# Optimization experiments

Measured on AMD Instinct MI355X. Metric: run time of the kernel, lower is better.

Reference implementation:

```python
import jax, jax.numpy as jnp
import numpy as np
import math

C = 256
NUM_GROUPS = 8
EPS = 1e-5


def group_norm(x, scale, bias):
    # x: (B, C, H, W)
    B, Cc, H, W = x.shape
    g = x.reshape(B, NUM_GROUPS, Cc // NUM_GROUPS, H, W)
    mean = g.mean(axis=(2, 3, 4), keepdims=True)
    var = g.var(axis=(2, 3, 4), keepdims=True)
    g = (g - mean) * jax.lax.rsqrt(var + EPS)
    x = g.reshape(B, Cc, H, W)
    return x * scale[None, :, None, None] + bias[None, :, None, None]


def setup_inputs() -> dict:
    key = jax.random.key(0)
    ks = jax.random.split(key, 6)
    B, H, W = 4, 64, 64
    s = 1.0 / math.sqrt(C)
    return {
        "input": jax.random.normal(ks[0], (B, C, H, W), dtype=jnp.float32),
        "gn_scale": jnp.ones((C,), jnp.float32),
        "gn_bias": jnp.zeros((C,), jnp.float32),
        "Wq": jax.random.normal(ks[1], (C, C), jnp.float32) * s,
        "bq": jnp.zeros((C,), jnp.float32),
        "Wk": jax.random.normal(ks[2], (C, C), jnp.float32) * s,
        "bk": jnp.zeros((C,), jnp.float32),
        "Wv": jax.random.normal(ks[3], (C, C), jnp.float32) * s,
        "bv": jnp.zeros((C,), jnp.float32),
        "Wo": jax.random.normal(ks[4], (C, C), jnp.float32) * s,
        "bo": jnp.zeros((C,), jnp.float32),
    }


def reference(input, gn_scale, gn_bias, Wq, bq, Wk, bk, Wv, bv, Wo, bo):
    B, Cc, H, W = input.shape
    N = H * W
    h = group_norm(input, gn_scale, gn_bias)          # (B,C,H,W)
    hf = h.reshape(B, Cc, N)                          # (B,C,N)
    # 1x1 convs are per-pixel linear maps: out[c] = W[c,c'] h[c'] + b[c]
    q = jnp.einsum('oc,bcn->bon', Wq, hf) + bq[None, :, None]
    k = jnp.einsum('oc,bcn->bon', Wk, hf) + bk[None, :, None]
    v = jnp.einsum('oc,bcn->bon', Wv, hf) + bv[None, :, None]
    # attention: scores (B,N,N) = q^T k / sqrt(C)
    attn = jnp.einsum('bcn,bcm->bnm', q, k) / jnp.sqrt(jnp.float32(Cc))
    attn = jax.nn.softmax(attn, axis=-1)
    # output = value @ attention^T -> (B,C,N)
    out = jnp.einsum('bcm,bnm->bcn', v, attn)
    out = out.reshape(B, Cc, H, W)
    out = jnp.einsum('oc,bchw->bohw', Wo, out) + bo[None, :, None, None]
    return input + out
```

## Files before the change

kernel.cpp:

```cpp
#include <hip/hip_runtime.h>
#include <hip/hip_bf16.h>
#include <stdint.h>

#define BATCH 4
#define CH 256
#define NPIX 4096
#define NGROUP 8
#define GCH 32
#define EPSV 1e-5f

typedef __attribute__((ext_vector_type(8))) short bf16x8;
typedef __attribute__((ext_vector_type(4))) float f32x4;
typedef __attribute__((ext_vector_type(16))) float f32x16;

#define MFMA_B16(a, b, c) __builtin_amdgcn_mfma_f32_16x16x32_bf16((a), (b), (c), 0, 0, 0)
#define MFMA32(a, b, c)   __builtin_amdgcn_mfma_f32_32x32x16_bf16((a), (b), (c), 0, 0, 0)

#define GLOAD16(gsrc, ldst)                                                        \
  __builtin_amdgcn_global_load_lds(                                               \
      (const __attribute__((address_space(1))) uint32_t*)(gsrc),                  \
      (__attribute__((address_space(3))) uint32_t*)(ldst), 16, 0, 0)

__device__ __forceinline__ unsigned short f2bf(float f) {
  union { float f; uint32_t u; } v; v.f = f;
  return (unsigned short)((v.u + 0x7FFFu + ((v.u >> 16) & 1u)) >> 16);
}
__device__ __forceinline__ float bf2f(unsigned short h) {
  union { uint32_t u; float f; } v; v.u = ((uint32_t)h) << 16;
  return v.f;
}

#define QSCALE 0.09016813306f

__global__ __launch_bounds__(256) void wconv(
    const float* __restrict__ Wq, const float* __restrict__ Wk,
    const float* __restrict__ Wv, const float* __restrict__ Wo,
    const float* __restrict__ bq,
    unsigned short* __restrict__ Wq_b, unsigned short* __restrict__ Wk_b,
    unsigned short* __restrict__ Wv_b, unsigned short* __restrict__ Wo_b,
    float* __restrict__ bq_s) {
  int i = blockIdx.x * 256 + threadIdx.x;
  Wq_b[i] = f2bf(Wq[i] * QSCALE);
  Wk_b[i] = f2bf(Wk[i]);
  Wv_b[i] = f2bf(Wv[i]);
  Wo_b[i] = f2bf(Wo[i]);
  if (i < CH) bq_s[i] = bq[i] * QSCALE;
}

__global__ __launch_bounds__(256) void gn_stats(const float* __restrict__ x,
                                                float* __restrict__ part) {
  int bc = blockIdx.x;
  const float* row = x + (size_t)bc * NPIX;
  int t = threadIdx.x;
  float s = 0.f, ss = 0.f;
  #pragma unroll
  for (int i = 0; i < 4; ++i) {
    f32x4 v = *(const f32x4*)(row + (i * 256 + t) * 4);
    s += v[0] + v[1] + v[2] + v[3];
    ss += v[0]*v[0] + v[1]*v[1] + v[2]*v[2] + v[3]*v[3];
  }
  #pragma unroll
  for (int m = 1; m < 64; m <<= 1) { s += __shfl_xor(s, m); ss += __shfl_xor(ss, m); }
  __shared__ float ls[8];
  if ((t & 63) == 0) { ls[(t >> 6) * 2] = s; ls[(t >> 6) * 2 + 1] = ss; }
  __syncthreads();
  if (t == 0) {
    part[bc * 2]     = ls[0] + ls[2] + ls[4] + ls[6];
    part[bc * 2 + 1] = ls[1] + ls[3] + ls[5] + ls[7];
  }
}

__global__ __launch_bounds__(256) void gn_apply(
    const float* __restrict__ x, const float* __restrict__ part,
    const float* __restrict__ gamma, const float* __restrict__ beta,
    unsigned short* __restrict__ h_t) {
  int chunk = blockIdx.x, g = blockIdx.y, b = blockIdx.z;
  int t = threadIdx.x;
  __shared__ float s_mean, s_rstd;
  __shared__ unsigned short tile[GCH][72];
  if (t == 0) {
    float S = 0.f, SS = 0.f;
    const float* p = part + (size_t)(b * CH + g * GCH) * 2;
    for (int j = 0; j < GCH; ++j) { S += p[2 * j]; SS += p[2 * j + 1]; }
    float inv = 1.0f / (float)(GCH * NPIX);
    float mean = S * inv;
    float var = SS * inv - mean * mean;
    s_mean = mean;
    s_rstd = rsqrtf(var + EPSV);
  }
  __syncthreads();
  float mean = s_mean, rstd = s_rstd;
  int n0 = chunk * 64;
  int p = t & 63;
  int csub = t >> 6;
  #pragma unroll
  for (int cl = 0; cl < GCH; cl += 4) {
    int c = cl + csub;
    float val = x[(size_t)(b * CH + g * GCH + c) * NPIX + n0 + p];
    float gm = gamma[g * GCH + c], bt = beta[g * GCH + c];
    tile[c][p] = f2bf((val - mean) * rstd * gm + bt);
  }
  __syncthreads();
  int pix = t >> 2, cc = (t & 3) * 8;
  bf16x8 vv;
  #pragma unroll
  for (int j = 0; j < 8; ++j) vv[j] = (short)tile[cc + j][pix];
  *(bf16x8*)(h_t + (size_t)(b * NPIX + n0 + pix) * CH + g * GCH + cc) = vv;
}

template <int BIAS_COL, int RESID, int OUT_BF16>
__global__ __launch_bounds__(256, 2) void gemm_bt_k(
    const unsigned short* __restrict__ A, const unsigned short* __restrict__ Bt,
    void* __restrict__ Cout, const float* __restrict__ bias,
    const float* __restrict__ resid, int M, int N,
    long aStride, long btStride, long cStride) {
  __shared__ __align__(16) unsigned short a_lds[128 * 64];
  __shared__ __align__(16) unsigned short b_lds[128 * 64];

  const int bz = blockIdx.z;
  const char* Ac = (const char*)(A + (size_t)bz * aStride);
  const char* Bc = (const char*)(Bt + (size_t)bz * btStride);
  const int m0 = blockIdx.x * 128;
  const int n0 = blockIdx.y * 128;
  const int t = threadIdx.x;
  const int w = t >> 6, l = t & 63, lr = l & 15, lk = l >> 4;
  const int wr = (w >> 1) * 64, wc = (w & 1) * 64;

  f32x4 acc[4][4];
  #pragma unroll
  for (int i = 0; i < 4; ++i)
    #pragma unroll
    for (int j = 0; j < 4; ++j) acc[i][j] = f32x4{0.f, 0.f, 0.f, 0.f};

  char* alc = (char*)a_lds;
  char* blc = (char*)b_lds;

  for (int kt = 0; kt < 4; ++kt) {
    __syncthreads();
    #pragma unroll
    for (int i = 0; i < 4; ++i) {
      int base = i * 4096 + w * 1024;
      int lin = base + l * 16;
      int sw = lin ^ (((lin >> 7) & 7) << 4);
      int row = lin >> 7;
      int inr = sw & 127;
      GLOAD16(Ac + (size_t)(m0 + row) * 512 + kt * 128 + inr, alc + base);
      GLOAD16(Bc + (size_t)(n0 + row) * 512 + kt * 128 + inr, blc + base);
    }
    __syncthreads();
    #pragma unroll
    for (int ks = 0; ks < 2; ++ks) {
      bf16x8 af[4], bf[4];
      #pragma unroll
      for (int f = 0; f < 4; ++f) {
        int ra = wr + f * 16 + lr;
        int la = ra * 128 + ks * 64 + lk * 16;
        af[f] = *(const bf16x8*)(alc + (la ^ ((ra & 7) << 4)));
        int rb = wc + f * 16 + lr;
        int lb = rb * 128 + ks * 64 + lk * 16;
        bf[f] = *(const bf16x8*)(blc + (lb ^ ((rb & 7) << 4)));
      }
      #pragma unroll
      for (int mf = 0; mf < 4; ++mf)
        #pragma unroll
        for (int nf = 0; nf < 4; ++nf)
          acc[mf][nf] = MFMA_B16(af[mf], bf[nf], acc[mf][nf]);
    }
  }

  #pragma unroll
  for (int mf = 0; mf < 4; ++mf) {
    #pragma unroll
    for (int nf = 0; nf < 4; ++nf) {
      int col = n0 + wc + nf * 16 + lr;
      #pragma unroll
      for (int r = 0; r < 4; ++r) {
        int row = m0 + wr + mf * 16 + lk * 4 + r;
        float val = acc[mf][nf][r];
        val += BIAS_COL ? bias[col] : bias[row];
        size_t idx = (size_t)bz * (size_t)cStride + (size_t)row * N + col;
        if (RESID) val += resid[idx];
        if (OUT_BF16) ((unsigned short*)Cout)[idx] = f2bf(val);
        else          ((float*)Cout)[idx] = val;
      }
    }
  }
}

#define KSPLIT 4
#define KRANGE (NPIX / KSPLIT)
#define KBLK 32
#define NT (KRANGE / KBLK)

__global__ __launch_bounds__(256, 2) void flash_kernel(
    const unsigned short* __restrict__ q_t, const unsigned short* __restrict__ k_t,
    const unsigned short* __restrict__ v,
    unsigned short* __restrict__ p0, unsigned short* __restrict__ p1,
    unsigned short* __restrict__ p2, unsigned short* __restrict__ p3,
    float* __restrict__ ml) {
  __shared__ __align__(16) unsigned short k_lds[2][KBLK * CH];
  __shared__ __align__(16) unsigned short v_lds[2][CH * KBLK];

  const int F = blockIdx.x;
  const int bid = (F >> 3) + ((F & 7) << 6);
  const int qx = bid & 31, b = (bid >> 5) & 3, ksp = bid >> 7;
  const int q0 = qx * 128;
  const int t = threadIdx.x;
  const int w = t >> 6, l = t & 63;
  const int l31 = l & 31, hi = l >> 5;

  bf16x8 qf[16];
  {
    const char* qp = (const char*)(q_t + (size_t)(b * NPIX + q0 + w * 32 + l31) * CH);
    #pragma unroll
    for (int ds = 0; ds < 16; ++ds)
      qf[ds] = *(const bf16x8*)(qp + ds * 32 + hi * 16);
  }

  f32x16 oacc[8];
  #pragma unroll
  for (int cf = 0; cf < 8; ++cf)
    #pragma unroll
    for (int r = 0; r < 16; ++r) oacc[cf][r] = 0.f;
  float m_run = -3e38f, l_run = 0.f;
  uint32_t pkc[8];
  #pragma unroll
  for (int m = 0; m < 8; ++m) pkc[m] = 0;

  const char* kg = (const char*)(k_t + ((size_t)b * NPIX + ksp * KRANGE) * CH);
  const char* vg = (const char*)(v + (size_t)b * CH * NPIX + ksp * KRANGE);

  int koffb[4], voffb[4], ldsd[4];
  #pragma unroll
  for (int i_ = 0; i_ < 4; ++i_) {
    int d = i_ * 4096 + w * 1024 + l * 16;
    ldsd[i_] = d;
    int r_ = d >> 9;
    int c_ = ((d >> 4) & 31) ^ r_;
    koffb[i_] = r_ * 512 + (c_ << 4);
    voffb[i_] = ((c_ >> 2) * 32 + r_) * (NPIX * 2) + ((c_ & 3) << 4);
  }

  #define STAGE_K(buf, tt)                                                         \
    { _Pragma("unroll")                                                            \
      for (int i_ = 0; i_ < 4; ++i_)                                               \
        GLOAD16(kg + (size_t)koffb[i_] + (size_t)(tt) * (KBLK * 512),              \
                (char*)k_lds[buf] + ldsd[i_]); }
  #define STAGE_V(buf, tt)                                                         \
    { _Pragma("unroll")                                                            \
      for (int i_ = 0; i_ < 4; ++i_)                                               \
        GLOAD16(vg + (size_t)voffb[i_] + (size_t)(tt) * (KBLK * 2),                \
                (char*)v_lds[buf] + ldsd[i_]); }

  auto do_pv = [&](const char* vlcx) {
    #pragma unroll
    for (int s = 0; s < 2; ++s) {
      uint32_t own0 = hi ? pkc[4 * s + 2] : pkc[4 * s + 0];
      uint32_t own1 = hi ? pkc[4 * s + 3] : pkc[4 * s + 1];
      uint32_t snd0 = hi ? pkc[4 * s + 0] : pkc[4 * s + 2];
      uint32_t snd1 = hi ? pkc[4 * s + 1] : pkc[4 * s + 3];
      uint32_t rcv0 = (uint32_t)__shfl_xor((int)snd0, 32);
      uint32_t rcv1 = (uint32_t)__shfl_xor((int)snd1, 32);
      union { uint32_t u[4]; bf16x8 v8; } apu;
      apu.u[0] = hi ? rcv0 : own0;
      apu.u[1] = hi ? rcv1 : own1;
      apu.u[2] = hi ? own0 : rcv0;
      apu.u[3] = hi ? own1 : rcv1;
      bf16x8 ap = apu.v8;
      #pragma unroll
      for (int cf = 0; cf < 8; ++cf) {
        bf16x8 bv = *(const bf16x8*)(
            vlcx + l31 * 512 + ((((cf << 2) + (s << 1) + hi) ^ l31) << 4));
        oacc[cf] = MFMA32(ap, bv, oacc[cf]);
      }
    }
  };

  STAGE_K(0, 0);
  STAGE_K(1, 1);
  STAGE_V(0, 0);
  asm volatile("s_waitcnt vmcnt(8)" ::: "memory");
  __builtin_amdgcn_s_barrier();

  for (int u = 0; u < NT; ++u) {
    const char* klc = (const char*)k_lds[u & 1];
    const char* vlc = (const char*)v_lds[(u ^ 1) & 1];

    __builtin_amdgcn_s_setprio(1);
    if (u > 0) do_pv(vlc);
    f32x16 sacc;
    #pragma unroll
    for (int r = 0; r < 16; ++r) sacc[r] = 0.f;
    #pragma unroll
    for (int ds = 0; ds < 16; ++ds) {
      bf16x8 kf = *(const bf16x8*)(klc + l31 * 512 + ((((ds << 1) + hi) ^ l31) << 4));
      sacc = MFMA32(kf, qf[ds], sacc);
    }
    __builtin_amdgcn_s_setprio(0);

    float mx[8];
    #pragma unroll
    for (int r = 0; r < 8; ++r) mx[r] = fmaxf(sacc[r], sacc[r + 8]);
    #pragma unroll
    for (int st = 4; st >= 1; st >>= 1)
      #pragma unroll
      for (int r = 0; r < 4; ++r)
        if (r < st) mx[r] = fmaxf(mx[r], mx[r + st]);
    float tm = fmaxf(mx[0], __shfl_xor(mx[0], 32));

    if (!__all(tm <= m_run + 6.f)) {
      float mn = fmaxf(m_run, tm);
      float al = exp2f(m_run - mn);
      m_run = mn;
      l_run *= al;
      #pragma unroll
      for (int r = 0; r < 16; ++r) {
        float alr = __shfl(al, (r & 3) + 8 * (r >> 2) + 4 * hi);
        #pragma unroll
        for (int cf = 0; cf < 8; ++cf) oacc[cf][r] *= alr;
      }
    }

    float psp[4] = {0.f, 0.f, 0.f, 0.f};
    #pragma unroll
    for (int m = 0; m < 8; ++m) {
      float pa = exp2f(sacc[2 * m] - m_run);
      float pb = exp2f(sacc[2 * m + 1] - m_run);
      psp[m & 3] += pa + pb;
      union { __hip_bfloat162 h2; uint32_t u; } cv;
      cv.h2 = __float22bfloat162_rn(make_float2(pa, pb));
      pkc[m] = cv.u;
    }
    float ps = (psp[0] + psp[1]) + (psp[2] + psp[3]);
    ps += __shfl_xor(ps, 32);
    l_run += ps;

    asm volatile("" ::: "memory");
    __builtin_amdgcn_s_barrier();
    if (u + 2 < NT) STAGE_K((u & 1), u + 2);
    if (u + 1 < NT) STAGE_V(((u + 1) & 1), u + 1);
    if (u + 2 < NT)      { asm volatile("s_waitcnt vmcnt(8)" ::: "memory"); }
    else if (u + 1 < NT) { asm volatile("s_waitcnt vmcnt(4)" ::: "memory"); }
    else                 { asm volatile("s_waitcnt vmcnt(0)" ::: "memory"); }
    __builtin_amdgcn_s_barrier();
  }

  __builtin_amdgcn_s_setprio(1);
  do_pv((const char*)v_lds[(NT - 1) & 1]);
  __builtin_amdgcn_s_setprio(0);

  {
    unsigned short* opart = (ksp == 0) ? p0 : (ksp == 1) ? p1 : (ksp == 2) ? p2 : p3;
    unsigned short* op = opart + (size_t)(b * NPIX + q0 + w * 32) * CH;
    #pragma unroll
    for (int cf = 0; cf < 8; ++cf)
      #pragma unroll
      for (int r = 0; r < 16; ++r)
        op[(size_t)((r & 3) + 8 * (r >> 2) + 4 * hi) * CH + cf * 32 + l31] =
            f2bf(oacc[cf][r]);
    if (l < 32) {
      float* mlrow = ml + ((size_t)ksp * (BATCH * NPIX) +
                           b * NPIX + q0 + w * 32 + l) * 2;
      mlrow[0] = m_run;
      mlrow[1] = l_run;
    }
  }
  #undef STAGE_K
  #undef STAGE_V
}

__global__ __launch_bounds__(256) void flash_merge(
    const unsigned short* __restrict__ p0, unsigned short* __restrict__ p1io,
    const unsigned short* __restrict__ p2, const unsigned short* __restrict__ p3,
    const float* __restrict__ ml) {
  const int R = BATCH * NPIX;
  int t = threadIdx.x;
  int gr = blockIdx.x * 16 + (t >> 4);
  int colg = (t & 15) * 16;
  float m0 = ml[(size_t)gr * 2],           l0 = ml[(size_t)gr * 2 + 1];
  float m1 = ml[((size_t)R + gr) * 2],     l1 = ml[((size_t)R + gr) * 2 + 1];
  float m2 = ml[((size_t)2 * R + gr) * 2], l2 = ml[((size_t)2 * R + gr) * 2 + 1];
  float m3 = ml[((size_t)3 * R + gr) * 2], l3 = ml[((size_t)3 * R + gr) * 2 + 1];
  float m = fmaxf(fmaxf(m0, m1), fmaxf(m2, m3));
  float e0 = exp2f(m0 - m), e1 = exp2f(m1 - m);
  float e2 = exp2f(m2 - m), e3 = exp2f(m3 - m);
  float inv = 1.0f / (e0 * l0 + e1 * l1 + e2 * l2 + e3 * l3);
  const bf16x8* a0 = (const bf16x8*)(p0 + (size_t)gr * CH + colg);
  bf16x8*       a1 = (bf16x8*)(p1io + (size_t)gr * CH + colg);
  const bf16x8* a2 = (const bf16x8*)(p2 + (size_t)gr * CH + colg);
  const bf16x8* a3 = (const bf16x8*)(p3 + (size_t)gr * CH + colg);
  #pragma unroll
  for (int h = 0; h < 2; ++h) {
    bf16x8 v0 = a0[h], v1 = a1[h], v2 = a2[h], v3 = a3[h], o;
    #pragma unroll
    for (int j = 0; j < 8; ++j)
      o[j] = (short)f2bf((e0 * bf2f((unsigned short)v0[j]) +
                          e1 * bf2f((unsigned short)v1[j]) +
                          e2 * bf2f((unsigned short)v2[j]) +
                          e3 * bf2f((unsigned short)v3[j])) * inv);
    a1[h] = o;
  }
}

extern "C" void kernel_launch(void* const* d_in, const int* in_sizes, int n_in,
                              void* d_out, int out_size, void* d_ws, size_t ws_size,
                              hipStream_t stream) {
  const float* x   = (const float*)d_in[0];
  const float* gsc = (const float*)d_in[1];
  const float* gbi = (const float*)d_in[2];
  const float* Wq  = (const float*)d_in[3];
  const float* bq  = (const float*)d_in[4];
  const float* Wk  = (const float*)d_in[5];
  const float* bk  = (const float*)d_in[6];
  const float* Wv  = (const float*)d_in[7];
  const float* bv  = (const float*)d_in[8];
  const float* Wo  = (const float*)d_in[9];
  const float* bo  = (const float*)d_in[10];

  char* ws = (char*)d_ws;
  unsigned short* Wq_b = (unsigned short*)(ws);
  unsigned short* Wk_b = (unsigned short*)(ws + 131072);
  unsigned short* Wv_b = (unsigned short*)(ws + 262144);
  unsigned short* Wo_b = (unsigned short*)(ws + 393216);
  float* bq_s          = (float*)(ws + 524288);
  float* part          = (float*)(ws + 525312);
  char* big            = ws + 533504;
  unsigned short* h_t  = (unsigned short*)(big);
  unsigned short* q_t  = (unsigned short*)(big + 1 * 8388608ull);
  unsigned short* k_t  = (unsigned short*)(big + 2 * 8388608ull);
  unsigned short* v_   = (unsigned short*)(big + 3 * 8388608ull);
  unsigned short* o_t  = (unsigned short*)(big + 4 * 8388608ull);
  float* ml            = (float*)(big + 5 * 8388608ull);
  if (ws_size < 533504 + 5ull * 8388608ull + 524288ull) return;

  unsigned short* dout_u = (unsigned short*)d_out;
  unsigned short* op2 = dout_u;
  unsigned short* op3 = dout_u + 4194304;

  wconv<<<256, 256, 0, stream>>>(Wq, Wk, Wv, Wo, bq, Wq_b, Wk_b, Wv_b, Wo_b, bq_s);
  gn_stats<<<BATCH * CH, 256, 0, stream>>>(x, part);
  gn_apply<<<dim3(64, NGROUP, BATCH), 256, 0, stream>>>(x, part, gsc, gbi, h_t);

  gemm_bt_k<1, 0, 1><<<dim3(128, 2, 1), 256, 0, stream>>>(
      h_t, Wq_b, q_t, bq_s, nullptr, 16384, 256, 0, 0, 0);
  gemm_bt_k<1, 0, 1><<<dim3(128, 2, 1), 256, 0, stream>>>(
      h_t, Wk_b, k_t, bk, nullptr, 16384, 256, 0, 0, 0);
  gemm_bt_k<0, 0, 1><<<dim3(2, 32, BATCH), 256, 0, stream>>>(
      Wv_b, h_t, v_, bv, nullptr, 256, 4096, 0, 1048576, 1048576);

  flash_kernel<<<dim3(32 * BATCH * KSPLIT, 1, 1), 256, 0, stream>>>(
      q_t, k_t, v_, h_t, o_t, op2, op3, ml);
  flash_merge<<<(BATCH * NPIX) / 16, 256, 0, stream>>>(h_t, o_t, op2, op3, ml);

  gemm_bt_k<0, 1, 0><<<dim3(2, 32, BATCH), 256, 0, stream>>>(
      Wo_b, o_t, (float*)d_out, bo, x, 256, 4096, 0, 1048576, 1048576);
}
```

Baseline: 146.7 us.

## Fuse Q and K projections into one GEMM and restructure flash loop

The Q and K projection GEMMs become a single launch over a 512-wide output whose epilogue splits columns between the q_t and k_t buffers. The bias is a concatenated scaled-q/k vector built in wconv. In the flash kernel, the per-lane swizzled LDS offsets are precomputed into registers. The main loop is unrolled by two with compile-time buffer indices, and the PV pass uses packed bf16 P fragments built at the end of each iteration rather than shuffling at the start of the next. This aims to cut one launch, reuse the A-tile reads of h_t, and reduce address arithmetic in the hot loop, at the cost of more live registers.

```diff
diff --git a/kernel.cpp b/kernel.cpp
--- a/kernel.cpp
+++ b/kernel.cpp
@@ -35,16 +35,19 @@
 __global__ __launch_bounds__(256) void wconv(
     const float* __restrict__ Wq, const float* __restrict__ Wk,
     const float* __restrict__ Wv, const float* __restrict__ Wo,
-    const float* __restrict__ bq,
+    const float* __restrict__ bq, const float* __restrict__ bk,
     unsigned short* __restrict__ Wq_b, unsigned short* __restrict__ Wk_b,
     unsigned short* __restrict__ Wv_b, unsigned short* __restrict__ Wo_b,
-    float* __restrict__ bq_s) {
+    float* __restrict__ bqk_s) {
   int i = blockIdx.x * 256 + threadIdx.x;
   Wq_b[i] = f2bf(Wq[i] * QSCALE);
   Wk_b[i] = f2bf(Wk[i]);
   Wv_b[i] = f2bf(Wv[i]);
   Wo_b[i] = f2bf(Wo[i]);
-  if (i < CH) bq_s[i] = bq[i] * QSCALE;
+  if (i < CH) {
+    bqk_s[i] = bq[i] * QSCALE;
+    bqk_s[CH + i] = bk[i];
+  }
 }
 
 __global__ __launch_bounds__(256) void gn_stats(const float* __restrict__ x,
@@ -108,12 +111,12 @@
   *(bf16x8*)(h_t + (size_t)(b * NPIX + n0 + pix) * CH + g * GCH + cc) = vv;
 }
 
-template <int BIAS_COL, int RESID, int OUT_BF16>
+template <int BIAS_COL, int RESID, int OUT_BF16, int SPLIT>
 __global__ __launch_bounds__(256, 2) void gemm_bt_k(
     const unsigned short* __restrict__ A, const unsigned short* __restrict__ Bt,
     void* __restrict__ Cout, const float* __restrict__ bias,
     const float* __restrict__ resid, int M, int N,
-    long aStride, long btStride, long cStride) {
+    long aStride, long btStride, long cStride, void* __restrict__ Cout2) {
   __shared__ __align__(16) unsigned short a_lds[128 * 64];
   __shared__ __align__(16) unsigned short b_lds[128 * 64];
 
@@ -178,10 +181,16 @@
         int row = m0 + wr + mf * 16 + lk * 4 + r;
         float val = acc[mf][nf][r];
         val += BIAS_COL ? bias[col] : bias[row];
-        size_t idx = (size_t)bz * (size_t)cStride + (size_t)row * N + col;
-        if (RESID) val += resid[idx];
-        if (OUT_BF16) ((unsigned short*)Cout)[idx] = f2bf(val);
-        else          ((float*)Cout)[idx] = val;
+        if (SPLIT) {
+          unsigned short* dst = (col < 256) ? (unsigned short*)Cout
+                                            : (unsigned short*)Cout2;
+          dst[(size_t)row * 256 + (col & 255)] = f2bf(val);
+        } else {
+          size_t idx = (size_t)bz * (size_t)cStride + (size_t)row * N + col;
+          if (RESID) val += resid[idx];
+          if (OUT_BF16) ((unsigned short*)Cout)[idx] = f2bf(val);
+          else          ((float*)Cout)[idx] = val;
+        }
       }
     }
   }
@@ -217,15 +226,18 @@
       qf[ds] = *(const bf16x8*)(qp + ds * 32 + hi * 16);
   }
 
+  uint32_t xoff[16];
+  #pragma unroll
+  for (int j = 0; j < 16; ++j)
+    xoff[j] = (uint32_t)(l31 * 512 + ((((j << 1) + hi) ^ l31) << 4));
+
   f32x16 oacc[8];
   #pragma unroll
   for (int cf = 0; cf < 8; ++cf)
     #pragma unroll
     for (int r = 0; r < 16; ++r) oacc[cf][r] = 0.f;
   float m_run = -3e38f, l_run = 0.f;
-  uint32_t pkc[8];
-  #pragma unroll
-  for (int m = 0; m < 8; ++m) pkc[m] = 0;
+  bf16x8 paf[2];
 
   const char* kg = (const char*)(k_t + ((size_t)b * NPIX + ksp * KRANGE) * CH);
   const char* vg = (const char*)(v + (size_t)b * CH * NPIX + ksp * KRANGE);
@@ -244,37 +256,99 @@
   #define STAGE_K(buf, tt)                                                         \
     { _Pragma("unroll")                                                            \
       for (int i_ = 0; i_ < 4; ++i_)                                               \
-        GLOAD16(kg + (size_t)koffb[i_] + (size_t)(tt) * (KBLK * 512),              \
+        GLOAD16(kg + (size_t)(koffb[i_] + (tt) * (KBLK * 512)),                    \
                 (char*)k_lds[buf] + ldsd[i_]); }
   #define STAGE_V(buf, tt)                                                         \
     { _Pragma("unroll")                                                            \
       for (int i_ = 0; i_ < 4; ++i_)                                               \
-        GLOAD16(vg + (size_t)voffb[i_] + (size_t)(tt) * (KBLK * 2),                \
+        GLOAD16(vg + (size_t)(voffb[i_] + (tt) * (KBLK * 2)),                      \
                 (char*)v_lds[buf] + ldsd[i_]); }
 
-  auto do_pv = [&](const char* vlcx) {
-    #pragma unroll
-    for (int s = 0; s < 2; ++s) {
-      uint32_t own0 = hi ? pkc[4 * s + 2] : pkc[4 * s + 0];
-      uint32_t own1 = hi ? pkc[4 * s + 3] : pkc[4 * s + 1];
-      uint32_t snd0 = hi ? pkc[4 * s + 0] : pkc[4 * s + 2];
-      uint32_t snd1 = hi ? pkc[4 * s + 1] : pkc[4 * s + 3];
-      uint32_t rcv0 = (uint32_t)__shfl_xor((int)snd0, 32);
-      uint32_t rcv1 = (uint32_t)__shfl_xor((int)snd1, 32);
-      union { uint32_t u[4]; bf16x8 v8; } apu;
-      apu.u[0] = hi ? rcv0 : own0;
-      apu.u[1] = hi ? rcv1 : own1;
-      apu.u[2] = hi ? own0 : rcv0;
-      apu.u[3] = hi ? own1 : rcv1;
-      bf16x8 ap = apu.v8;
-      #pragma unroll
-      for (int cf = 0; cf < 8; ++cf) {
-        bf16x8 bv = *(const bf16x8*)(
-            vlcx + l31 * 512 + ((((cf << 2) + (s << 1) + hi) ^ l31) << 4));
-        oacc[cf] = MFMA32(ap, bv, oacc[cf]);
-      }
-    }
-  };
+  #define ITER(P, uu)                                                              \
+  {                                                                                \
+    const char* klc = (const char*)k_lds[(P)];                                     \
+    const char* vlc = (const char*)v_lds[(P) ^ 1];                                 \
+    __builtin_amdgcn_s_setprio(1);                                                 \
+    if ((uu) > 0) {            \
+      _Pragma("unroll")                                                            \
+      for (int s = 0; s < 2; ++s) {                                                \
+        _Pragma("unroll")                                                          \
+        for (int cf = 0; cf < 8; ++cf) {                                           \
+          bf16x8 bv = *(const bf16x8*)(vlc + xoff[cf * 2 + s]);                    \
+          oacc[cf] = MFMA32(paf[s], bv, oacc[cf]);                                 \
+        }                                                                          \
+      }                                                                            \
+    }                                                                              \
+    f32x16 sacc;                                                                   \
+    _Pragma("unroll")                                                              \
+    for (int r = 0; r < 16; ++r) sacc[r] = 0.f;                                    \
+    _Pragma("unroll")                                                              \
+    for (int ds = 0; ds < 16; ++ds) {                                              \
+      bf16x8 kf = *(const bf16x8*)(klc + xoff[ds]);                                \
+      sacc = MFMA32(kf, qf[ds], sacc);                                             \
+    }                                                                              \
+    __builtin_amdgcn_s_setprio(0);                                                 \
+                                              \
+    float p8[8];                                                                   \
+    _Pragma("unroll")                                                              \
+    for (int r = 0; r < 8; ++r) p8[r] = fmaxf(sacc[r], sacc[r + 8]);               \
+    float ta = fmaxf(fmaxf(p8[0], p8[1]), p8[2]);                                  \
+    float tb = fmaxf(fmaxf(p8[3], p8[4]), p8[5]);                                  \
+    float tc = fmaxf(fmaxf(p8[6], p8[7]), ta);                                     \
+    float tmx = fmaxf(tb, tc);                                                     \
+    tmx = fmaxf(tmx, __shfl_xor(tmx, 32));                                         \
+    if (!__all(tmx <= m_run + 6.f)) {                   \
+      float mn = fmaxf(m_run, tmx);                                                \
+      float al = exp2f(m_run - mn);                                                \
+      m_run = mn;                                                                  \
+      l_run *= al;                                                                 \
+      _Pragma("unroll")                                                            \
+      for (int r = 0; r < 16; ++r) {                                               \
+        float alr = __shfl(al, (r & 3) + 8 * (r >> 2) + 4 * hi);                   \
+        _Pragma("unroll")                                                          \
+        for (int cf = 0; cf < 8; ++cf) oacc[cf][r] *= alr;                         \
+      }                                                                            \
+    }                                                                              \
+    uint32_t pkc[8];                                                               \
+    float q8[8];                                                                   \
+    _Pragma("unroll")                                                              \
+    for (int m = 0; m < 8; ++m) {                                                  \
+      float pa = exp2f(sacc[2 * m] - m_run);                                       \
+      float pb = exp2f(sacc[2 * m + 1] - m_run);                                   \
+      q8[m] = pa + pb;                                                             \
+      union { __hip_bfloat162 h2; uint32_t u; } cv;                                \
+      cv.h2 = __float22bfloat162_rn(make_float2(pa, pb));                          \
+      pkc[m] = cv.u;                                                               \
+    }                                                                              \
+    float ps = ((q8[0] + q8[1]) + (q8[2] + q8[3])) +                               \
+               ((q8[4] + q8[5]) + (q8[6] + q8[7]));                                \
+    ps += __shfl_xor(ps, 32);                                                      \
+    l_run += ps;                                                                   \
+          \
+    _Pragma("unroll")                                                              \
+    for (int s = 0; s < 2; ++s) {                                                  \
+      uint32_t own0 = hi ? pkc[4 * s + 2] : pkc[4 * s + 0];                        \
+      uint32_t own1 = hi ? pkc[4 * s + 3] : pkc[4 * s + 1];                        \
+      uint32_t snd0 = hi ? pkc[4 * s + 0] : pkc[4 * s + 2];                        \
+      uint32_t snd1 = hi ? pkc[4 * s + 1] : pkc[4 * s + 3];                        \
+      uint32_t rcv0 = (uint32_t)__shfl_xor((int)snd0, 32);                         \
+      uint32_t rcv1 = (uint32_t)__shfl_xor((int)snd1, 32);                         \
+      union { uint32_t u[4]; bf16x8 v8; } apu;                                     \
+      apu.u[0] = hi ? rcv0 : own0;                                                 \
+      apu.u[1] = hi ? rcv1 : own1;                                                 \
+      apu.u[2] = hi ? own0 : rcv0;                                                 \
+      apu.u[3] = hi ? own1 : rcv1;                                                 \
+      paf[s] = apu.v8;                                                             \
+    }                                                                              \
+    asm volatile("" ::: "memory");                                                 \
+    __builtin_amdgcn_s_barrier();      \
+    if ((uu) + 2 < NT) STAGE_K((P), (uu) + 2);                                     \
+    if ((uu) + 1 < NT) STAGE_V((P) ^ 1, (uu) + 1);                                 \
+    if ((uu) + 2 < NT)      { asm volatile("s_waitcnt vmcnt(8)" ::: "memory"); }   \
+    else if ((uu) + 1 < NT) { asm volatile("s_waitcnt vmcnt(4)" ::: "memory"); }   \
+    else                    { asm volatile("s_waitcnt vmcnt(0)" ::: "memory"); }   \
+    __builtin_amdgcn_s_barrier();         \
+  }
 
   STAGE_K(0, 0);
   STAGE_K(1, 1);
@@ -282,71 +356,23 @@
   asm volatile("s_waitcnt vmcnt(8)" ::: "memory");
   __builtin_amdgcn_s_barrier();
 
-  for (int u = 0; u < NT; ++u) {
-    const char* klc = (const char*)k_lds[u & 1];
-    const char* vlc = (const char*)v_lds[(u ^ 1) & 1];
-
-    __builtin_amdgcn_s_setprio(1);
-    if (u > 0) do_pv(vlc);
-    f32x16 sacc;
-    #pragma unroll
-    for (int r = 0; r < 16; ++r) sacc[r] = 0.f;
-    #pragma unroll
-    for (int ds = 0; ds < 16; ++ds) {
-      bf16x8 kf = *(const bf16x8*)(klc + l31 * 512 + ((((ds << 1) + hi) ^ l31) << 4));
-      sacc = MFMA32(kf, qf[ds], sacc);
-    }
-    __builtin_amdgcn_s_setprio(0);
-
-    float mx[8];
-    #pragma unroll
-    for (int r = 0; r < 8; ++r) mx[r] = fmaxf(sacc[r], sacc[r + 8]);
-    #pragma unroll
-    for (int st = 4; st >= 1; st >>= 1)
+  for (int u = 0; u < NT; u += 2) {
+    ITER(0, u);
+    ITER(1, u + 1);
+  }
+
+  __builtin_amdgcn_s_setprio(1);
+  {
+    const char* vlc = (const char*)v_lds[1];
+    #pragma unroll
+    for (int s = 0; s < 2; ++s) {
       #pragma unroll
-      for (int r = 0; r < 4; ++r)
-        if (r < st) mx[r] = fmaxf(mx[r], mx[r + st]);
-    float tm = fmaxf(mx[0], __shfl_xor(mx[0], 32));
-
-    if (!__all(tm <= m_run + 6.f)) {
-      float mn = fmaxf(m_run, tm);
-      float al = exp2f(m_run - mn);
-      m_run = mn;
-      l_run *= al;
-      #pragma unroll
-      for (int r = 0; r < 16; ++r) {
-        float alr = __shfl(al, (r & 3) + 8 * (r >> 2) + 4 * hi);
-        #pragma unroll
-        for (int cf = 0; cf < 8; ++cf) oacc[cf][r] *= alr;
+      for (int cf = 0; cf < 8; ++cf) {
+        bf16x8 bv = *(const bf16x8*)(vlc + xoff[cf * 2 + s]);
+        oacc[cf] = MFMA32(paf[s], bv, oacc[cf]);
       }
     }
-
-    float psp[4] = {0.f, 0.f, 0.f, 0.f};
-    #pragma unroll
-    for (int m = 0; m < 8; ++m) {
-      float pa = exp2f(sacc[2 * m] - m_run);
-      float pb = exp2f(sacc[2 * m + 1] - m_run);
-      psp[m & 3] += pa + pb;
-      union { __hip_bfloat162 h2; uint32_t u; } cv;
-      cv.h2 = __float22bfloat162_rn(make_float2(pa, pb));
-      pkc[m] = cv.u;
-    }
-    float ps = (psp[0] + psp[1]) + (psp[2] + psp[3]);
-    ps += __shfl_xor(ps, 32);
-    l_run += ps;
-
-    asm volatile("" ::: "memory");
-    __builtin_amdgcn_s_barrier();
-    if (u + 2 < NT) STAGE_K((u & 1), u + 2);
-    if (u + 1 < NT) STAGE_V(((u + 1) & 1), u + 1);
-    if (u + 2 < NT)      { asm volatile("s_waitcnt vmcnt(8)" ::: "memory"); }
-    else if (u + 1 < NT) { asm volatile("s_waitcnt vmcnt(4)" ::: "memory"); }
-    else                 { asm volatile("s_waitcnt vmcnt(0)" ::: "memory"); }
-    __builtin_amdgcn_s_barrier();
-  }
-
-  __builtin_amdgcn_s_setprio(1);
-  do_pv((const char*)v_lds[(NT - 1) & 1]);
+  }
   __builtin_amdgcn_s_setprio(0);
 
   {
@@ -365,6 +391,7 @@
       mlrow[1] = l_run;
     }
   }
+  #undef ITER
   #undef STAGE_K
   #undef STAGE_V
 }
@@ -422,36 +449,35 @@
   unsigned short* Wk_b = (unsigned short*)(ws + 131072);
   unsigned short* Wv_b = (unsigned short*)(ws + 262144);
   unsigned short* Wo_b = (unsigned short*)(ws + 393216);
-  float* bq_s          = (float*)(ws + 524288);
-  float* part          = (float*)(ws + 525312);
-  char* big            = ws + 533504;
+  float* bqk_s         = (float*)(ws + 524288);
+  float* part          = (float*)(ws + 526336);
+  char* big            = ws + 534528;
   unsigned short* h_t  = (unsigned short*)(big);
   unsigned short* q_t  = (unsigned short*)(big + 1 * 8388608ull);
   unsigned short* k_t  = (unsigned short*)(big + 2 * 8388608ull);
   unsigned short* v_   = (unsigned short*)(big + 3 * 8388608ull);
   unsigned short* o_t  = (unsigned short*)(big + 4 * 8388608ull);
   float* ml            = (float*)(big + 5 * 8388608ull);
-  if (ws_size < 533504 + 5ull * 8388608ull + 524288ull) return;
+  if (ws_size < 534528 + 5ull * 8388608ull + 524288ull) return;
 
   unsigned short* dout_u = (unsigned short*)d_out;
   unsigned short* op2 = dout_u;
   unsigned short* op3 = dout_u + 4194304;
 
-  wconv<<<256, 256, 0, stream>>>(Wq, Wk, Wv, Wo, bq, Wq_b, Wk_b, Wv_b, Wo_b, bq_s);
+  wconv<<<256, 256, 0, stream>>>(Wq, Wk, Wv, Wo, bq, bk,
+                                 Wq_b, Wk_b, Wv_b, Wo_b, bqk_s);
   gn_stats<<<BATCH * CH, 256, 0, stream>>>(x, part);
   gn_apply<<<dim3(64, NGROUP, BATCH), 256, 0, stream>>>(x, part, gsc, gbi, h_t);
 
-  gemm_bt_k<1, 0, 1><<<dim3(128, 2, 1), 256, 0, stream>>>(
-      h_t, Wq_b, q_t, bq_s, nullptr, 16384, 256, 0, 0, 0);
-  gemm_bt_k<1, 0, 1><<<dim3(128, 2, 1), 256, 0, stream>>>(
-      h_t, Wk_b, k_t, bk, nullptr, 16384, 256, 0, 0, 0);
-  gemm_bt_k<0, 0, 1><<<dim3(2, 32, BATCH), 256, 0, stream>>>(
-      Wv_b, h_t, v_, bv, nullptr, 256, 4096, 0, 1048576, 1048576);
+  gemm_bt_k<1, 0, 1, 1><<<dim3(128, 4, 1), 256, 0, stream>>>(
+      h_t, Wq_b, q_t, bqk_s, nullptr, 16384, 512, 0, 0, 0, k_t);
+  gemm_bt_k<0, 0, 1, 0><<<dim3(2, 32, BATCH), 256, 0, stream>>>(
+      Wv_b, h_t, v_, bv, nullptr, 256, 4096, 0, 1048576, 1048576, nullptr);
 
   flash_kernel<<<dim3(32 * BATCH * KSPLIT, 1, 1), 256, 0, stream>>>(
       q_t, k_t, v_, h_t, o_t, op2, op3, ml);
   flash_merge<<<(BATCH * NPIX) / 16, 256, 0, stream>>>(h_t, o_t, op2, op3, ml);
 
-  gemm_bt_k<0, 1, 0><<<dim3(2, 32, BATCH), 256, 0, stream>>>(
-      Wo_b, o_t, (float*)d_out, bo, x, 256, 4096, 0, 1048576, 1048576);
-}
+  gemm_bt_k<0, 1, 0, 0><<<dim3(2, 32, BATCH), 256, 0, stream>>>(
+      Wo_b, o_t, (float*)d_out, bo, x, 256, 4096, 0, 1048576, 1048576, nullptr);
+}
```

Result: slower. 157.3 us (+7.2%).

## Fuse Q/K projection GEMMs and single-buffer V tile to raise flash occupancy

Applied to the files above, without the earlier changes.

The Q and K projections become one GEMM launch with N=512. It relies on Wq_b and Wk_b being contiguous in the workspace, and the epilogue routes each column half to q_t or k_t using a concatenated bias array. This removes a launch and a second pass over h_t. Separately, the flash kernel drops V double-buffering to cut LDS use and raises launch bounds to 3 blocks per CU. V is now loaded each iteration after the barrier, so its load is less hidden behind QK compute.

```diff
diff --git a/kernel.cpp b/kernel.cpp
--- a/kernel.cpp
+++ b/kernel.cpp
@@ -35,16 +35,19 @@
 __global__ __launch_bounds__(256) void wconv(
     const float* __restrict__ Wq, const float* __restrict__ Wk,
     const float* __restrict__ Wv, const float* __restrict__ Wo,
-    const float* __restrict__ bq,
+    const float* __restrict__ bq, const float* __restrict__ bk,
     unsigned short* __restrict__ Wq_b, unsigned short* __restrict__ Wk_b,
     unsigned short* __restrict__ Wv_b, unsigned short* __restrict__ Wo_b,
-    float* __restrict__ bq_s) {
+    float* __restrict__ bqk_s) {
   int i = blockIdx.x * 256 + threadIdx.x;
   Wq_b[i] = f2bf(Wq[i] * QSCALE);
   Wk_b[i] = f2bf(Wk[i]);
   Wv_b[i] = f2bf(Wv[i]);
   Wo_b[i] = f2bf(Wo[i]);
-  if (i < CH) bq_s[i] = bq[i] * QSCALE;
+  if (i < CH) {
+    bqk_s[i] = bq[i] * QSCALE;
+    bqk_s[CH + i] = bk[i];
+  }
 }
 
 __global__ __launch_bounds__(256) void gn_stats(const float* __restrict__ x,
@@ -108,12 +111,12 @@
   *(bf16x8*)(h_t + (size_t)(b * NPIX + n0 + pix) * CH + g * GCH + cc) = vv;
 }
 
-template <int BIAS_COL, int RESID, int OUT_BF16>
+template <int BIAS_COL, int RESID, int OUT_BF16, int SPLIT>
 __global__ __launch_bounds__(256, 2) void gemm_bt_k(
     const unsigned short* __restrict__ A, const unsigned short* __restrict__ Bt,
     void* __restrict__ Cout, const float* __restrict__ bias,
     const float* __restrict__ resid, int M, int N,
-    long aStride, long btStride, long cStride) {
+    long aStride, long btStride, long cStride, void* __restrict__ Cout2) {
   __shared__ __align__(16) unsigned short a_lds[128 * 64];
   __shared__ __align__(16) unsigned short b_lds[128 * 64];
 
@@ -178,10 +181,16 @@
         int row = m0 + wr + mf * 16 + lk * 4 + r;
         float val = acc[mf][nf][r];
         val += BIAS_COL ? bias[col] : bias[row];
-        size_t idx = (size_t)bz * (size_t)cStride + (size_t)row * N + col;
-        if (RESID) val += resid[idx];
-        if (OUT_BF16) ((unsigned short*)Cout)[idx] = f2bf(val);
-        else          ((float*)Cout)[idx] = val;
+        if (SPLIT) {
+          unsigned short* dst = (col < 256) ? (unsigned short*)Cout
+                                            : (unsigned short*)Cout2;
+          dst[(size_t)row * 256 + (col & 255)] = f2bf(val);
+        } else {
+          size_t idx = (size_t)bz * (size_t)cStride + (size_t)row * N + col;
+          if (RESID) val += resid[idx];
+          if (OUT_BF16) ((unsigned short*)Cout)[idx] = f2bf(val);
+          else          ((float*)Cout)[idx] = val;
+        }
       }
     }
   }
@@ -192,14 +201,14 @@
 #define KBLK 32
 #define NT (KRANGE / KBLK)
 
-__global__ __launch_bounds__(256, 2) void flash_kernel(
+__global__ __launch_bounds__(256, 3) void flash_kernel(
     const unsigned short* __restrict__ q_t, const unsigned short* __restrict__ k_t,
     const unsigned short* __restrict__ v,
     unsigned short* __restrict__ p0, unsigned short* __restrict__ p1,
     unsigned short* __restrict__ p2, unsigned short* __restrict__ p3,
     float* __restrict__ ml) {
   __shared__ __align__(16) unsigned short k_lds[2][KBLK * CH];
-  __shared__ __align__(16) unsigned short v_lds[2][CH * KBLK];
+  __shared__ __align__(16) unsigned short v_lds[CH * KBLK];
 
   const int F = blockIdx.x;
   const int bid = (F >> 3) + ((F & 7) << 6);
@@ -244,13 +253,13 @@
   #define STAGE_K(buf, tt)                                                         \
     { _Pragma("unroll")                                                            \
       for (int i_ = 0; i_ < 4; ++i_)                                               \
-        GLOAD16(kg + (size_t)koffb[i_] + (size_t)(tt) * (KBLK * 512),              \
+        GLOAD16(kg + (size_t)(koffb[i_] + (tt) * (KBLK * 512)),                    \
                 (char*)k_lds[buf] + ldsd[i_]); }
-  #define STAGE_V(buf, tt)                                                         \
+  #define STAGE_V(tt)                                                              \
     { _Pragma("unroll")                                                            \
       for (int i_ = 0; i_ < 4; ++i_)                                               \
-        GLOAD16(vg + (size_t)voffb[i_] + (size_t)(tt) * (KBLK * 2),                \
-                (char*)v_lds[buf] + ldsd[i_]); }
+        GLOAD16(vg + (size_t)(voffb[i_] + (tt) * (KBLK * 2)),                      \
+                (char*)v_lds + ldsd[i_]); }
 
   auto do_pv = [&](const char* vlcx) {
     #pragma unroll
@@ -278,16 +287,14 @@
 
   STAGE_K(0, 0);
   STAGE_K(1, 1);
-  STAGE_V(0, 0);
-  asm volatile("s_waitcnt vmcnt(8)" ::: "memory");
+  asm volatile("s_waitcnt vmcnt(4)" ::: "memory");
   __builtin_amdgcn_s_barrier();
 
   for (int u = 0; u < NT; ++u) {
     const char* klc = (const char*)k_lds[u & 1];
-    const char* vlc = (const char*)v_lds[(u ^ 1) & 1];
 
     __builtin_amdgcn_s_setprio(1);
-    if (u > 0) do_pv(vlc);
+    if (u > 0) do_pv((const char*)v_lds);
     f32x16 sacc;
     #pragma unroll
     for (int r = 0; r < 16; ++r) sacc[r] = 0.f;
@@ -337,16 +344,15 @@
 
     asm volatile("" ::: "memory");
     __builtin_amdgcn_s_barrier();
+    STAGE_V(u);
     if (u + 2 < NT) STAGE_K((u & 1), u + 2);
-    if (u + 1 < NT) STAGE_V(((u + 1) & 1), u + 1);
-    if (u + 2 < NT)      { asm volatile("s_waitcnt vmcnt(8)" ::: "memory"); }
-    else if (u + 1 < NT) { asm volatile("s_waitcnt vmcnt(4)" ::: "memory"); }
-    else                 { asm volatile("s_waitcnt vmcnt(0)" ::: "memory"); }
+    if (u + 2 < NT) { asm volatile("s_waitcnt vmcnt(4)" ::: "memory"); }
+    else            { asm volatile("s_waitcnt vmcnt(0)" ::: "memory"); }
     __builtin_amdgcn_s_barrier();
   }
 
   __builtin_amdgcn_s_setprio(1);
-  do_pv((const char*)v_lds[(NT - 1) & 1]);
+  do_pv((const char*)v_lds);
   __builtin_amdgcn_s_setprio(0);
 
   {
@@ -422,36 +428,35 @@
   unsigned short* Wk_b = (unsigned short*)(ws + 131072);
   unsigned short* Wv_b = (unsigned short*)(ws + 262144);
   unsigned short* Wo_b = (unsigned short*)(ws + 393216);
-  float* bq_s          = (float*)(ws + 524288);
-  float* part          = (float*)(ws + 525312);
-  char* big            = ws + 533504;
+  float* bqk_s         = (float*)(ws + 524288);
+  float* part          = (float*)(ws + 526336);
+  char* big            = ws + 534528;
   unsigned short* h_t  = (unsigned short*)(big);
   unsigned short* q_t  = (unsigned short*)(big + 1 * 8388608ull);
   unsigned short* k_t  = (unsigned short*)(big + 2 * 8388608ull);
   unsigned short* v_   = (unsigned short*)(big + 3 * 8388608ull);
   unsigned short* o_t  = (unsigned short*)(big + 4 * 8388608ull);
   float* ml            = (float*)(big + 5 * 8388608ull);
-  if (ws_size < 533504 + 5ull * 8388608ull + 524288ull) return;
+  if (ws_size < 534528 + 5ull * 8388608ull + 524288ull) return;
 
   unsigned short* dout_u = (unsigned short*)d_out;
   unsigned short* op2 = dout_u;
   unsigned short* op3 = dout_u + 4194304;
 
-  wconv<<<256, 256, 0, stream>>>(Wq, Wk, Wv, Wo, bq, Wq_b, Wk_b, Wv_b, Wo_b, bq_s);
+  wconv<<<256, 256, 0, stream>>>(Wq, Wk, Wv, Wo, bq, bk,
+                                 Wq_b, Wk_b, Wv_b, Wo_b, bqk_s);
   gn_stats<<<BATCH * CH, 256, 0, stream>>>(x, part);
   gn_apply<<<dim3(64, NGROUP, BATCH), 256, 0, stream>>>(x, part, gsc, gbi, h_t);
 
-  gemm_bt_k<1, 0, 1><<<dim3(128, 2, 1), 256, 0, stream>>>(
-      h_t, Wq_b, q_t, bq_s, nullptr, 16384, 256, 0, 0, 0);
-  gemm_bt_k<1, 0, 1><<<dim3(128, 2, 1), 256, 0, stream>>>(
-      h_t, Wk_b, k_t, bk, nullptr, 16384, 256, 0, 0, 0);
-  gemm_bt_k<0, 0, 1><<<dim3(2, 32, BATCH), 256, 0, stream>>>(
-      Wv_b, h_t, v_, bv, nullptr, 256, 4096, 0, 1048576, 1048576);
+  gemm_bt_k<1, 0, 1, 1><<<dim3(128, 4, 1), 256, 0, stream>>>(
+      h_t, Wq_b, q_t, bqk_s, nullptr, 16384, 512, 0, 0, 0, k_t);
+  gemm_bt_k<0, 0, 1, 0><<<dim3(2, 32, BATCH), 256, 0, stream>>>(
+      Wv_b, h_t, v_, bv, nullptr, 256, 4096, 0, 1048576, 1048576, nullptr);
 
   flash_kernel<<<dim3(32 * BATCH * KSPLIT, 1, 1), 256, 0, stream>>>(
       q_t, k_t, v_, h_t, o_t, op2, op3, ml);
   flash_merge<<<(BATCH * NPIX) / 16, 256, 0, stream>>>(h_t, o_t, op2, op3, ml);
 
-  gemm_bt_k<0, 1, 0><<<dim3(2, 32, BATCH), 256, 0, stream>>>(
-      Wo_b, o_t, (float*)d_out, bo, x, 256, 4096, 0, 1048576, 1048576);
-}
+  gemm_bt_k<0, 1, 0, 0><<<dim3(2, 32, BATCH), 256, 0, stream>>>(
+      Wo_b, o_t, (float*)d_out, bo, x, 256, 4096, 0, 1048576, 1048576, nullptr);
+}
```

Result: slower. 525.5 us (+258.2%).
